# Kernel tuning notes

Measured on AMD Instinct MI355X. Metric: run time of the kernel, lower is better.

Reference implementation:

```python
import jax, jax.numpy as jnp
import numpy as np

B, T, Z, S, H = 32, 128, 100, 6, 64
F1, F2 = 512, 128


def setup_inputs() -> dict:
    key = jax.random.key(0)
    ks = jax.random.split(key, 11)
    g = lambda k, shape, sc: (jax.random.normal(k, shape, dtype=jnp.float32) * sc)
    return {
        "x": jax.random.normal(ks[0], (B, T, Z, S), dtype=jnp.float32),
        "W_ih": g(ks[1], (3 * H, S), 0.125),   # GRU input weights [r|z|n]
        "W_hh": g(ks[2], (3 * H, H), 0.125),   # GRU hidden weights [r|z|n]
        "b_ih": g(ks[3], (3 * H,), 0.125),
        "b_hh": g(ks[4], (3 * H,), 0.125),
        "w1": g(ks[5], (F1, H), 0.1),
        "b1": g(ks[6], (F1,), 0.1),
        "w2": g(ks[7], (F2, F1), 0.04),
        "b2": g(ks[8], (F2,), 0.04),
        "w3": g(ks[9], (1, F2), 0.09),
        "b3": g(ks[10], (1,), 0.09),
    }


def reference(x, W_ih, W_hh, b_ih, b_hh, w1, b1, w2, b2, w3, b3):
    b, t, z, s = x.shape
    h_dim = W_hh.shape[1]
    # Fuse the per-zone python loop into the batch dim, zone-major so the
    # final reshape matches torch.stack(a).view(-1, t, nzones).
    xm = jnp.transpose(x, (2, 0, 1, 3)).reshape(z * b, t, s)  # (ZB, T, S)
    # Precompute input projections for all timesteps (one big GEMM).
    gi_all = jnp.einsum('nts,gs->ntg', xm, W_ih) + b_ih        # (ZB, T, 3H)

    def step(h, gi):
        gh = h @ W_hh.T + b_hh
        r = jax.nn.sigmoid(gi[:, :h_dim] + gh[:, :h_dim])
        zg = jax.nn.sigmoid(gi[:, h_dim:2 * h_dim] + gh[:, h_dim:2 * h_dim])
        n = jnp.tanh(gi[:, 2 * h_dim:] + r * gh[:, 2 * h_dim:])
        h_new = (1.0 - zg) * n + zg * h
        return h_new, h_new

    h0 = jnp.zeros((z * b, h_dim), x.dtype)
    _, sx = jax.lax.scan(step, h0, jnp.swapaxes(gi_all, 0, 1))  # (T, ZB, H)
    sx = jnp.swapaxes(sx, 0, 1)                                  # (ZB, T, H)

    a1 = jax.nn.relu(sx @ w1.T + b1)
    a2 = jax.nn.relu(a1 @ w2.T + b2)
    a3 = a2 @ w3.T + b3                                          # (ZB, T, 1)
    return a3.reshape(-1, t, z)                                  # (B, T, Z)
```

## Files before the change

kernel.cpp:

```cpp
#include <hip/hip_runtime.h>
#include <stdint.h>

#define Tdim 128
#define Zdim 100
#define Sdim 6
#define Hdim 64
#define ZB   3200
#define F1   512
#define F2   128
#define Mrows (ZB * Tdim)

typedef _Float16 f16x8 __attribute__((ext_vector_type(8)));
typedef _Float16 f16x4 __attribute__((ext_vector_type(4)));
typedef float f32x4 __attribute__((ext_vector_type(4)));
typedef uint32_t u32x4 __attribute__((ext_vector_type(4)));

__device__ __forceinline__ float sigmoidf_fast(float x) {
  return 1.f / (1.f + __expf(-x));
}
__device__ __forceinline__ float tanhf_fast(float x) {
  return 1.f - 2.f / (__expf(2.f * x) + 1.f);
}

__global__ __launch_bounds__(256) void prep_kernel(
    const float* __restrict__ W_ih, const float* __restrict__ W_hh,
    const float* __restrict__ w1, const float* __restrict__ w2,
    _Float16* __restrict__ Wf, _Float16* __restrict__ w1p,
    _Float16* __restrict__ w2p) {
  int i = blockIdx.x * 256 + threadIdx.x;
  if (i < 192 * 96) {
    int g = i / 96, k = i - g * 96;
    float v = (k < 64) ? W_hh[g * 64 + k] : ((k < 70) ? W_ih[g * 6 + (k - 64)] : 0.f);
    Wf[i] = (_Float16)v;
  }
  int j = i - 192 * 96;
  if (j >= 0 && j < 32768) {
    int kt = j >> 11, ntl = (j >> 10) & 1, kf = (j >> 9) & 1;
    int lane = (j >> 3) & 63, e = j & 7;
    int q = lane >> 4, c = lane & 15;
    int row = kt * 32 + ntl * 16 + c;
    int h = kf * 32 + q * 8 + e;
    w1p[j] = (_Float16)w1[row * 64 + h];
  }
  int l = j - 32768;
  if (l >= 0 && l < 65536) {
    int kt = l >> 12, nt = (l >> 9) & 7;
    int lane = (l >> 3) & 63, e = l & 7;
    int q = lane >> 4, c = lane & 15;
    int row = nt * 16 + c;
    int k = kt * 32 + q * 8 + e;
    w2p[l] = (_Float16)w2[row * 512 + k];
  }
}

__global__ __launch_bounds__(256, 1) void gru_kernel(
    const float* __restrict__ x, const _Float16* __restrict__ Wf,
    const float* __restrict__ b_ih, const float* __restrict__ b_hh,
    _Float16* __restrict__ sx) {
  __shared__ __align__(16) _Float16 hist[32][16][72];
  __shared__ __align__(16) _Float16 xs[Tdim][16][8];
  const int tid = threadIdx.x;
  const int lane = tid & 63;
  const int w = tid >> 6;
  const int c = lane & 15;
  const int q = lane >> 4;

  for (int i = 0; i < 8; i++) {
    int idx = i * 256 + tid;
    int t = idx >> 4, row = idx & 15;
    int nr = blockIdx.x * 16 + row;
    const float* p = x + (size_t)(nr & 31) * (Tdim * Zdim * Sdim)
                       + (size_t)t * (Zdim * Sdim) + (size_t)(nr >> 5) * Sdim;
    f16x8 v;
    v[0] = (_Float16)p[0]; v[1] = (_Float16)p[1]; v[2] = (_Float16)p[2];
    v[3] = (_Float16)p[3]; v[4] = (_Float16)p[4]; v[5] = (_Float16)p[5];
    v[6] = (_Float16)0.f;  v[7] = (_Float16)0.f;
    *(f16x8*)&xs[t][row][0] = v;
  }

  const int gr0 = w * 16;
  const int gz0 = 64 + w * 16;
  const int gn0 = 128 + w * 16;

  f16x8 Ar[3], Az[3], Anh[2], Ani;
#pragma unroll
  for (int kf = 0; kf < 3; kf++) {
    Ar[kf] = *(const f16x8*)(Wf + (size_t)(gr0 + c) * 96 + kf * 32 + q * 8);
    Az[kf] = *(const f16x8*)(Wf + (size_t)(gz0 + c) * 96 + kf * 32 + q * 8);
  }
  Anh[0] = *(const f16x8*)(Wf + (size_t)(gn0 + c) * 96 + q * 8);
  Anh[1] = *(const f16x8*)(Wf + (size_t)(gn0 + c) * 96 + 32 + q * 8);
  Ani    = *(const f16x8*)(Wf + (size_t)(gn0 + c) * 96 + 64 + q * 8);

  f32x4 Cr, Cz, Cnh, Cni;
  {
    f32x4 bir = *(const f32x4*)(b_ih + gr0 + q * 4);
    f32x4 bhr = *(const f32x4*)(b_hh + gr0 + q * 4);
    f32x4 biz = *(const f32x4*)(b_ih + gz0 + q * 4);
    f32x4 bhz = *(const f32x4*)(b_hh + gz0 + q * 4);
#pragma unroll
    for (int r = 0; r < 4; r++) { Cr[r] = bir[r] + bhr[r]; Cz[r] = biz[r] + bhz[r]; }
    Cnh = *(const f32x4*)(b_hh + gn0 + q * 4);
    Cni = *(const f32x4*)(b_ih + gn0 + q * 4);
  }

  __syncthreads();

  f16x8 Bh0 = {0, 0, 0, 0, 0, 0, 0, 0};
  f16x8 Bh1 = {0, 0, 0, 0, 0, 0, 0, 0};
  f32x4 hprev = {0.f, 0.f, 0.f, 0.f};

#pragma unroll 1
  for (int tch = 0; tch < 4; tch++) {
#pragma unroll 1
    for (int tc = 0; tc < 32; tc++) {
      const int t = tch * 32 + tc;
      f16x8 xv8 = *(const f16x8*)&xs[t][c][0];
      f16x8 Bx;
#pragma unroll
      for (int j = 0; j < 8; j++) Bx[j] = (q == 0) ? xv8[j] : (_Float16)0.f;

      f32x4 Dni = __builtin_amdgcn_mfma_f32_16x16x32_f16(Ani, Bx, Cni, 0, 0, 0);
      f32x4 Dr  = __builtin_amdgcn_mfma_f32_16x16x32_f16(Ar[2], Bx, Cr, 0, 0, 0);
      f32x4 Dz  = __builtin_amdgcn_mfma_f32_16x16x32_f16(Az[2], Bx, Cz, 0, 0, 0);
      f32x4 Dnh = __builtin_amdgcn_mfma_f32_16x16x32_f16(Anh[0], Bh0, Cnh, 0, 0, 0);
      Dr  = __builtin_amdgcn_mfma_f32_16x16x32_f16(Ar[0], Bh0, Dr, 0, 0, 0);
      Dz  = __builtin_amdgcn_mfma_f32_16x16x32_f16(Az[0], Bh0, Dz, 0, 0, 0);
      Dnh = __builtin_amdgcn_mfma_f32_16x16x32_f16(Anh[1], Bh1, Dnh, 0, 0, 0);
      Dr  = __builtin_amdgcn_mfma_f32_16x16x32_f16(Ar[1], Bh1, Dr, 0, 0, 0);
      Dz  = __builtin_amdgcn_mfma_f32_16x16x32_f16(Az[1], Bh1, Dz, 0, 0, 0);

      f16x4 pk;
#pragma unroll
      for (int r = 0; r < 4; r++) {
        float rr = sigmoidf_fast(Dr[r]);
        float zg = sigmoidf_fast(Dz[r]);
        float nn = tanhf_fast(Dni[r] + rr * Dnh[r]);
        float hnew = nn + zg * (hprev[r] - nn);
        hprev[r] = hnew;
        pk[r] = (_Float16)hnew;
      }
      *(f16x4*)&hist[tc][c][w * 16 + q * 4] = pk;
      __syncthreads();
      Bh0 = *(const f16x8*)&hist[tc][c][q * 8];
      Bh1 = *(const f16x8*)&hist[tc][c][32 + q * 8];
    }
    {
      const int t0 = tch * 32;
#pragma unroll
      for (int rr2 = 0; rr2 < 4; rr2++) {
        const int row = w * 4 + rr2;
        const int nrow = blockIdx.x * 16 + row;
        _Float16* dst = sx + (size_t)nrow * Tdim * Hdim + (size_t)t0 * Hdim;
#pragma unroll
        for (int it = 0; it < 4; it++) {
          int idx = it * 64 + lane;
          int tcc = idx >> 3, hd8 = idx & 7;
          f16x8 vv = *(const f16x8*)&hist[tcc][row][hd8 * 8];
          *(f16x8*)(dst + tcc * 64 + hd8 * 8) = vv;
        }
      }
      __syncthreads();
    }
  }
}

__global__ __launch_bounds__(256, 3) void mlp_kernel(
    const _Float16* __restrict__ sx, const _Float16* __restrict__ w1p,
    const _Float16* __restrict__ w2p, const float* __restrict__ b1,
    const float* __restrict__ b2, const float* __restrict__ w3,
    const float* __restrict__ b3, float* __restrict__ out) {
  __shared__ __align__(16) _Float16 w1s[2][2048];
  __shared__ __align__(16) _Float16 w2s[2][4096];
  __shared__ __align__(16) _Float16 rep[4][2][2][512];
  const int tid = threadIdx.x;
  const int lane = tid & 63;
  const int wave = tid >> 6;
  const int c = lane & 15;
  const int q = lane >> 4;
  const size_t m0 = ((size_t)blockIdx.x * 4 + wave) * 32;

  f16x8 Bs[2][2];
#pragma unroll
  for (int g = 0; g < 2; g++)
#pragma unroll
    for (int kk = 0; kk < 2; kk++)
      Bs[g][kk] = *(const f16x8*)(sx + (m0 + g * 16 + c) * Hdim + kk * 32 + q * 8);

  f32x4 acc2[2][8];
#pragma unroll
  for (int g = 0; g < 2; g++)
#pragma unroll
    for (int nt = 0; nt < 8; nt++) acc2[g][nt] = (f32x4){0.f, 0.f, 0.f, 0.f};

  u32x4 r1, r2a, r2b;
  {
    const u32x4* g1 = (const u32x4*)(w1p);
    const u32x4* g2 = (const u32x4*)(w2p);
    r1 = g1[tid];
    r2a = g2[tid];
    r2b = g2[256 + tid];
    ((u32x4*)&w1s[0][0])[tid] = r1;
    ((u32x4*)&w2s[0][0])[tid] = r2a;
    ((u32x4*)&w2s[0][0])[256 + tid] = r2b;
  }
  __syncthreads();

#pragma unroll 2
  for (int kt = 0; kt < 16; kt++) {
    const int buf = kt & 1;
    if (kt + 1 < 16) {
      const u32x4* g1 = (const u32x4*)(w1p + (size_t)(kt + 1) * 2048);
      const u32x4* g2 = (const u32x4*)(w2p + (size_t)(kt + 1) * 4096);
      r1 = g1[tid];
      r2a = g2[tid];
      r2b = g2[256 + tid];
    }

#pragma unroll
    for (int ntl = 0; ntl < 2; ntl++) {
      const int f1b = kt * 32 + ntl * 16;
      f16x8 A0 = *(const f16x8*)&w1s[buf][ntl * 1024 + lane * 8];
      f16x8 A1 = *(const f16x8*)&w1s[buf][ntl * 1024 + 512 + lane * 8];
      f32x4 bb = *(const f32x4*)(b1 + f1b + q * 4);
      const int roff = ((2 * ntl + (q >> 1)) * 16 + c) * 8 + (q & 1) * 4;
#pragma unroll
      for (int g = 0; g < 2; g++) {
        f32x4 cc = {0.f, 0.f, 0.f, 0.f};
        cc = __builtin_amdgcn_mfma_f32_16x16x32_f16(A0, Bs[g][0], cc, 0, 0, 0);
        cc = __builtin_amdgcn_mfma_f32_16x16x32_f16(A1, Bs[g][1], cc, 0, 0, 0);
        f16x4 pk;
#pragma unroll
        for (int r = 0; r < 4; r++) {
          float v = cc[r] + bb[r];
          pk[r] = (_Float16)(v > 0.f ? v : 0.f);
        }
        *(f16x4*)&rep[wave][buf][g][roff] = pk;
      }
    }
    f16x8 Ba[2];
#pragma unroll
    for (int g = 0; g < 2; g++)
      Ba[g] = *(const f16x8*)&rep[wave][buf][g][lane * 8];
#pragma unroll
    for (int nt = 0; nt < 8; nt++) {
      f16x8 A2 = *(const f16x8*)&w2s[buf][nt * 512 + lane * 8];
#pragma unroll
      for (int g = 0; g < 2; g++)
        acc2[g][nt] = __builtin_amdgcn_mfma_f32_16x16x32_f16(A2, Ba[g], acc2[g][nt], 0, 0, 0);
    }

    if (kt + 1 < 16) {
      ((u32x4*)&w1s[buf ^ 1][0])[tid] = r1;
      ((u32x4*)&w2s[buf ^ 1][0])[tid] = r2a;
      ((u32x4*)&w2s[buf ^ 1][0])[256 + tid] = r2b;
      __syncthreads();
    }
  }

  float part[2] = {0.f, 0.f};
#pragma unroll
  for (int nt = 0; nt < 8; nt++) {
    f32x4 bb = *(const f32x4*)(b2 + nt * 16 + q * 4);
    f32x4 ww = *(const f32x4*)(w3 + nt * 16 + q * 4);
#pragma unroll
    for (int g = 0; g < 2; g++) {
#pragma unroll
      for (int r = 0; r < 4; r++) {
        float v = acc2[g][nt][r] + bb[r];
        v = v > 0.f ? v : 0.f;
        part[g] = fmaf(v, ww[r], part[g]);
      }
    }
  }
#pragma unroll
  for (int g = 0; g < 2; g++) {
    part[g] += __shfl_xor(part[g], 16, 64);
    part[g] += __shfl_xor(part[g], 32, 64);
  }
  if (q < 2) {
    float pv = (q == 0) ? part[0] : part[1];
    out[m0 + q * 16 + c] = pv + b3[0];
  }
}

extern "C" void kernel_launch(void* const* d_in, const int* in_sizes, int n_in,
                              void* d_out, int out_size, void* d_ws, size_t ws_size,
                              hipStream_t stream) {
  const float* x    = (const float*)d_in[0];
  const float* W_ih = (const float*)d_in[1];
  const float* W_hh = (const float*)d_in[2];
  const float* b_ih = (const float*)d_in[3];
  const float* b_hh = (const float*)d_in[4];
  const float* w1   = (const float*)d_in[5];
  const float* b1   = (const float*)d_in[6];
  const float* w2   = (const float*)d_in[7];
  const float* b2   = (const float*)d_in[8];
  const float* w3   = (const float*)d_in[9];
  const float* b3   = (const float*)d_in[10];
  float* out = (float*)d_out;

  char* ws = (char*)d_ws;
  _Float16* sxf = (_Float16*)ws;
  _Float16* Wf  = (_Float16*)(ws + 52428800);
  _Float16* w1p = (_Float16*)(ws + 52428800 + 36864);
  _Float16* w2p = (_Float16*)(ws + 52428800 + 36864 + 65536);

  hipLaunchKernelGGL(prep_kernel, dim3(456), dim3(256), 0, stream,
                     W_ih, W_hh, w1, w2, Wf, w1p, w2p);
  hipLaunchKernelGGL(gru_kernel, dim3(ZB / 16), dim3(256), 0, stream,
                     x, Wf, b_ih, b_hh, sxf);
  hipLaunchKernelGGL(mlp_kernel, dim3(Mrows / 128), dim3(256), 0, stream,
                     sxf, w1p, w2p, b1, b2, w3, b3, out);
}
```

Baseline: 257.4 us.

## Prefetch next-step input projection in GRU and double MLP rows per wave

```diff
diff --git a/kernel.cpp b/kernel.cpp
--- a/kernel.cpp
+++ b/kernel.cpp
@@ -110,22 +110,25 @@
   f16x8 Bh1 = {0, 0, 0, 0, 0, 0, 0, 0};
   f32x4 hprev = {0.f, 0.f, 0.f, 0.f};
 
+  f32x4 Dr_s, Dz_s, Dni_s;
+  {
+    f16x8 xv8 = *(const f16x8*)&xs[0][c][0];
+    f16x8 Bx;
+#pragma unroll
+    for (int j = 0; j < 8; j++) Bx[j] = (q == 0) ? xv8[j] : (_Float16)0.f;
+    Dni_s = __builtin_amdgcn_mfma_f32_16x16x32_f16(Ani, Bx, Cni, 0, 0, 0);
+    Dr_s  = __builtin_amdgcn_mfma_f32_16x16x32_f16(Ar[2], Bx, Cr, 0, 0, 0);
+    Dz_s  = __builtin_amdgcn_mfma_f32_16x16x32_f16(Az[2], Bx, Cz, 0, 0, 0);
+  }
+
 #pragma unroll 1
   for (int tch = 0; tch < 4; tch++) {
 #pragma unroll 1
     for (int tc = 0; tc < 32; tc++) {
       const int t = tch * 32 + tc;
-      f16x8 xv8 = *(const f16x8*)&xs[t][c][0];
-      f16x8 Bx;
-#pragma unroll
-      for (int j = 0; j < 8; j++) Bx[j] = (q == 0) ? xv8[j] : (_Float16)0.f;
-
-      f32x4 Dni = __builtin_amdgcn_mfma_f32_16x16x32_f16(Ani, Bx, Cni, 0, 0, 0);
-      f32x4 Dr  = __builtin_amdgcn_mfma_f32_16x16x32_f16(Ar[2], Bx, Cr, 0, 0, 0);
-      f32x4 Dz  = __builtin_amdgcn_mfma_f32_16x16x32_f16(Az[2], Bx, Cz, 0, 0, 0);
       f32x4 Dnh = __builtin_amdgcn_mfma_f32_16x16x32_f16(Anh[0], Bh0, Cnh, 0, 0, 0);
-      Dr  = __builtin_amdgcn_mfma_f32_16x16x32_f16(Ar[0], Bh0, Dr, 0, 0, 0);
-      Dz  = __builtin_amdgcn_mfma_f32_16x16x32_f16(Az[0], Bh0, Dz, 0, 0, 0);
+      f32x4 Dr  = __builtin_amdgcn_mfma_f32_16x16x32_f16(Ar[0], Bh0, Dr_s, 0, 0, 0);
+      f32x4 Dz  = __builtin_amdgcn_mfma_f32_16x16x32_f16(Az[0], Bh0, Dz_s, 0, 0, 0);
       Dnh = __builtin_amdgcn_mfma_f32_16x16x32_f16(Anh[1], Bh1, Dnh, 0, 0, 0);
       Dr  = __builtin_amdgcn_mfma_f32_16x16x32_f16(Ar[1], Bh1, Dr, 0, 0, 0);
       Dz  = __builtin_amdgcn_mfma_f32_16x16x32_f16(Az[1], Bh1, Dz, 0, 0, 0);
@@ -135,12 +138,22 @@
       for (int r = 0; r < 4; r++) {
         float rr = sigmoidf_fast(Dr[r]);
         float zg = sigmoidf_fast(Dz[r]);
-        float nn = tanhf_fast(Dni[r] + rr * Dnh[r]);
+        float nn = tanhf_fast(Dni_s[r] + rr * Dnh[r]);
         float hnew = nn + zg * (hprev[r] - nn);
         hprev[r] = hnew;
         pk[r] = (_Float16)hnew;
       }
       *(f16x4*)&hist[tc][c][w * 16 + q * 4] = pk;
+
+      if (t + 1 < Tdim) {
+        f16x8 xv8 = *(const f16x8*)&xs[t + 1][c][0];
+        f16x8 Bx;
+#pragma unroll
+        for (int j = 0; j < 8; j++) Bx[j] = (q == 0) ? xv8[j] : (_Float16)0.f;
+        Dni_s = __builtin_amdgcn_mfma_f32_16x16x32_f16(Ani, Bx, Cni, 0, 0, 0);
+        Dr_s  = __builtin_amdgcn_mfma_f32_16x16x32_f16(Ar[2], Bx, Cr, 0, 0, 0);
+        Dz_s  = __builtin_amdgcn_mfma_f32_16x16x32_f16(Az[2], Bx, Cz, 0, 0, 0);
+      }
       __syncthreads();
       Bh0 = *(const f16x8*)&hist[tc][c][q * 8];
       Bh1 = *(const f16x8*)&hist[tc][c][32 + q * 8];
@@ -165,31 +178,31 @@
   }
 }
 
-__global__ __launch_bounds__(256, 3) void mlp_kernel(
+__global__ __launch_bounds__(256, 2) void mlp_kernel(
     const _Float16* __restrict__ sx, const _Float16* __restrict__ w1p,
     const _Float16* __restrict__ w2p, const float* __restrict__ b1,
     const float* __restrict__ b2, const float* __restrict__ w3,
     const float* __restrict__ b3, float* __restrict__ out) {
   __shared__ __align__(16) _Float16 w1s[2][2048];
   __shared__ __align__(16) _Float16 w2s[2][4096];
-  __shared__ __align__(16) _Float16 rep[4][2][2][512];
+  __shared__ __align__(16) _Float16 rep[4][4][512];
   const int tid = threadIdx.x;
   const int lane = tid & 63;
   const int wave = tid >> 6;
   const int c = lane & 15;
   const int q = lane >> 4;
-  const size_t m0 = ((size_t)blockIdx.x * 4 + wave) * 32;
-
-  f16x8 Bs[2][2];
-#pragma unroll
-  for (int g = 0; g < 2; g++)
+  const size_t m0 = ((size_t)blockIdx.x * 4 + wave) * 64;
+
+  f16x8 Bs[4][2];
+#pragma unroll
+  for (int g = 0; g < 4; g++)
 #pragma unroll
     for (int kk = 0; kk < 2; kk++)
       Bs[g][kk] = *(const f16x8*)(sx + (m0 + g * 16 + c) * Hdim + kk * 32 + q * 8);
 
-  f32x4 acc2[2][8];
-#pragma unroll
-  for (int g = 0; g < 2; g++)
+  f32x4 acc2[4][8];
+#pragma unroll
+  for (int g = 0; g < 4; g++)
 #pragma unroll
     for (int nt = 0; nt < 8; nt++) acc2[g][nt] = (f32x4){0.f, 0.f, 0.f, 0.f};
 
@@ -206,7 +219,7 @@
   }
   __syncthreads();
 
-#pragma unroll 2
+#pragma unroll 1
   for (int kt = 0; kt < 16; kt++) {
     const int buf = kt & 1;
     if (kt + 1 < 16) {
@@ -225,28 +238,25 @@
       f32x4 bb = *(const f32x4*)(b1 + f1b + q * 4);
       const int roff = ((2 * ntl + (q >> 1)) * 16 + c) * 8 + (q & 1) * 4;
 #pragma unroll
-      for (int g = 0; g < 2; g++) {
-        f32x4 cc = {0.f, 0.f, 0.f, 0.f};
-        cc = __builtin_amdgcn_mfma_f32_16x16x32_f16(A0, Bs[g][0], cc, 0, 0, 0);
+      for (int g = 0; g < 4; g++) {
+        f32x4 cc = __builtin_amdgcn_mfma_f32_16x16x32_f16(A0, Bs[g][0], bb, 0, 0, 0);
         cc = __builtin_amdgcn_mfma_f32_16x16x32_f16(A1, Bs[g][1], cc, 0, 0, 0);
         f16x4 pk;
 #pragma unroll
-        for (int r = 0; r < 4; r++) {
-          float v = cc[r] + bb[r];
-          pk[r] = (_Float16)(v > 0.f ? v : 0.f);
-        }
-        *(f16x4*)&rep[wave][buf][g][roff] = pk;
-      }
-    }
-    f16x8 Ba[2];
-#pragma unroll
-    for (int g = 0; g < 2; g++)
-      Ba[g] = *(const f16x8*)&rep[wave][buf][g][lane * 8];
+        for (int r = 0; r < 4; r++)
+          pk[r] = (_Float16)(cc[r] > 0.f ? cc[r] : 0.f);
+        *(f16x4*)&rep[wave][g][roff] = pk;
+      }
+    }
+    f16x8 Ba[4];
+#pragma unroll
+    for (int g = 0; g < 4; g++)
+      Ba[g] = *(const f16x8*)&rep[wave][g][lane * 8];
 #pragma unroll
     for (int nt = 0; nt < 8; nt++) {
       f16x8 A2 = *(const f16x8*)&w2s[buf][nt * 512 + lane * 8];
 #pragma unroll
-      for (int g = 0; g < 2; g++)
+      for (int g = 0; g < 4; g++)
         acc2[g][nt] = __builtin_amdgcn_mfma_f32_16x16x32_f16(A2, Ba[g], acc2[g][nt], 0, 0, 0);
     }
 
@@ -258,13 +268,13 @@
     }
   }
 
-  float part[2] = {0.f, 0.f};
+  float part[4] = {0.f, 0.f, 0.f, 0.f};
 #pragma unroll
   for (int nt = 0; nt < 8; nt++) {
     f32x4 bb = *(const f32x4*)(b2 + nt * 16 + q * 4);
     f32x4 ww = *(const f32x4*)(w3 + nt * 16 + q * 4);
 #pragma unroll
-    for (int g = 0; g < 2; g++) {
+    for (int g = 0; g < 4; g++) {
 #pragma unroll
       for (int r = 0; r < 4; r++) {
         float v = acc2[g][nt][r] + bb[r];
@@ -274,14 +284,12 @@
     }
   }
 #pragma unroll
-  for (int g = 0; g < 2; g++) {
+  for (int g = 0; g < 4; g++) {
     part[g] += __shfl_xor(part[g], 16, 64);
     part[g] += __shfl_xor(part[g], 32, 64);
   }
-  if (q < 2) {
-    float pv = (q == 0) ? part[0] : part[1];
-    out[m0 + q * 16 + c] = pv + b3[0];
-  }
+  float pv = (q == 0) ? part[0] : (q == 1) ? part[1] : (q == 2) ? part[2] : part[3];
+  out[m0 + q * 16 + c] = pv + b3[0];
 }
 
 extern "C" void kernel_launch(void* const* d_in, const int* in_sizes, int n_in,
@@ -310,6 +318,6 @@
                      W_ih, W_hh, w1, w2, Wf, w1p, w2p);
   hipLaunchKernelGGL(gru_kernel, dim3(ZB / 16), dim3(256), 0, stream,
                      x, Wf, b_ih, b_hh, sxf);
-  hipLaunchKernelGGL(mlp_kernel, dim3(Mrows / 128), dim3(256), 0, stream,
+  hipLaunchKernelGGL(mlp_kernel, dim3(Mrows / 256), dim3(256), 0, stream,
                      sxf, w1p, w2p, b1, b2, w3, b3, out);
 }
```

New measurement: 255.0 us. No clear change (-0.9%).
